# Optimization experiments

Measured on AMD Instinct MI355X. Metric: run time of the kernel, lower is better.

## Reference

```python
import jax, jax.numpy as jnp
import numpy as np

N_PRIORS = 125
N_CLASSES = 21
BATCH = 16384
THRESHOLD = 0.3
NEG_POS_RATIO = 3
ALPHA = 1.0


def setup_inputs() -> dict:
    key = jax.random.key(0)
    k1, k2, k3, k4, k5, k6, k7, k8 = jax.random.split(key, 8)
    predicted_locs = jax.random.normal(k1, (BATCH, N_PRIORS, 6), dtype=jnp.float32) * 0.1
    predicted_scores = jax.random.normal(k2, (BATCH, N_PRIORS, N_CLASSES), dtype=jnp.float32)
    # target: (N, 1, 8) = [cx, cy, w, h, angle, sin(a), cos(a), label]
    cxcy = jax.random.uniform(k3, (BATCH, 2), minval=0.2, maxval=0.8)
    wh = jax.random.uniform(k4, (BATCH, 2), minval=0.05, maxval=0.3)
    ang = jax.random.uniform(k5, (BATCH, 1), minval=-3.14159, maxval=3.14159)
    labels = jax.random.randint(k6, (BATCH, 1), 1, N_CLASSES).astype(jnp.float32)
    target = jnp.concatenate([cxcy, wh, ang, jnp.sin(ang), jnp.cos(ang), labels], axis=1)[:, None, :]
    # priors in cxcywh
    pc = jax.random.uniform(k7, (N_PRIORS, 2), minval=0.1, maxval=0.9)
    pwh = jax.random.uniform(k8, (N_PRIORS, 2), minval=0.05, maxval=0.4)
    priors_cxcy = jnp.concatenate([pc, pwh], axis=1)
    return {"predicted_locs": predicted_locs, "predicted_scores": predicted_scores,
            "target": target, "priors_cxcy": priors_cxcy}


def _iou_cxcywh(box, priors):
    # box: (4,), priors: (P,4) in (cx,cy,w,h); axis-aligned IoU
    b_lo = box[:2] - box[2:] * 0.5
    b_hi = box[:2] + box[2:] * 0.5
    p_lo = priors[:, :2] - priors[:, 2:] * 0.5
    p_hi = priors[:, :2] + priors[:, 2:] * 0.5
    inter_wh = jnp.clip(jnp.minimum(b_hi, p_hi) - jnp.maximum(b_lo, p_lo), 0.0)
    inter = inter_wh[:, 0] * inter_wh[:, 1]
    area_b = box[2] * box[3]
    area_p = priors[:, 2] * priors[:, 3]
    return inter / (area_b + area_p - inter)


def _cxcy_to_gcxgcy(cxcy, priors):
    # standard SSD encoding: cxcy (...,4) vs priors (P,4)
    g_cxcy = (cxcy[..., :2] - priors[:, :2]) / (priors[:, 2:] / 10.0)
    g_wh = jnp.log(cxcy[..., 2:] / priors[:, 2:]) * 5.0
    return jnp.concatenate([g_cxcy, g_wh], axis=-1)


def reference(predicted_locs, predicted_scores, target, priors_cxcy):
    P = priors_cxcy.shape[0]
    pred_angles = predicted_locs[..., 4:]   # (N,P,2)
    pred_locs = predicted_locs[..., :4]     # (N,P,4)

    def match(t):  # t: (1, 8), single object per image (n_objects = 1)
        box = t[0, :4]
        ov = _iou_cxcywh(box, priors_cxcy)                 # (P,)
        best_prior = jnp.argmax(ov)                        # prior_for_each_object
        ov = ov.at[best_prior].set(1.0)                    # force-match best prior
        label = jnp.where(ov < THRESHOLD, 0, t[0, 7].astype(jnp.int32))  # (P,)
        true_loc = _cxcy_to_gcxgcy(jnp.broadcast_to(box, (P, 4)), priors_cxcy)
        true_ang = jnp.broadcast_to(t[0, 5:7], (P, 2))
        return true_loc, label, true_ang

    true_locs, true_classes, true_angles = jax.vmap(match)(target)

    pos = true_classes != 0                                # (N,P)
    n_pos = pos.sum(axis=1)                                # (N,)
    n_pos_total = n_pos.sum().astype(jnp.float32)
    posf = pos.astype(jnp.float32)

    # smooth L1 (beta=1), mean over positive elements (4 coords each)
    d = pred_locs - true_locs
    sl1 = jnp.where(jnp.abs(d) < 1.0, 0.5 * d * d, jnp.abs(d) - 0.5)
    loc_loss = (sl1 * posf[..., None]).sum() / (n_pos_total * 4.0)

    # MSE over positive angle pairs, scaled by 25
    da = pred_angles - true_angles
    angle_loss = 25.0 * (da * da * posf[..., None]).sum() / (n_pos_total * 2.0)

    # per-prior cross entropy
    lse = jax.nn.logsumexp(predicted_scores, axis=-1)      # (N,P)
    picked = jnp.take_along_axis(predicted_scores, true_classes[..., None], axis=-1)[..., 0]
    conf_all = lse - picked                                # (N,P)

    conf_pos_sum = (conf_all * posf).sum()
    conf_neg = jnp.where(pos, 0.0, conf_all)
    conf_neg_sorted = -jnp.sort(-conf_neg, axis=1)         # descending
    ranks = jnp.arange(P)[None, :]
    hard = ranks < (NEG_POS_RATIO * n_pos)[:, None]
    conf_hard_neg_sum = (conf_neg_sorted * hard.astype(jnp.float32)).sum()
    conf_loss = (conf_hard_neg_sum + conf_pos_sum) / n_pos_total

    total = conf_loss + ALPHA * loc_loss + angle_loss
    return jnp.stack([conf_loss, loc_loss, angle_loss, total])
```

## Files before the change

kernel.cpp:

```cpp
#include <hip/hip_runtime.h>
#include <math.h>

#define NP 125
#define NC 21
#define ROWF (NP * NC)
#define THRESH 0.3f

__device__ inline void ald16(const float* g, float* l) {
    __builtin_amdgcn_global_load_lds(
        (const __attribute__((address_space(1))) void*)g,
        (__attribute__((address_space(3))) void*)l, 16, 0, 0);
}
__device__ inline void ald4(const float* g, float* l) {
    __builtin_amdgcn_global_load_lds(
        (const __attribute__((address_space(1))) void*)g,
        (__attribute__((address_space(3))) void*)l, 4, 0, 0);
}

__global__ void __launch_bounds__(64) mbloss_main(
    const float* __restrict__ locs, const float* __restrict__ scores,
    const float* __restrict__ target, const float* __restrict__ priors,
    float4* __restrict__ partials) {

    __shared__ float s_sc[ROWF];

    const int lane = threadIdx.x;
    const int r    = blockIdx.x;

    const float* gsc = scores + (size_t)r * ROWF;
#pragma unroll
    for (int it = 0; it < 10; ++it) {
        const int off = it * 256 + lane * 4;
        ald16(gsc + off, s_sc + off);
    }
    ald4(gsc + 2560 + lane, s_sc + 2560 + lane);
    if (lane == 0) s_sc[2624] = gsc[2624];

    const float* t = target + (size_t)r * 8;
    const float bx = t[0], by = t[1], bw = t[2], bh = t[3];
    const float sa = t[5], ca = t[6];
    const int lblT = (int)t[7];

    const int  p1 = lane + 64;
    const bool v1 = (p1 < NP);
    const float4* pr4 = (const float4*)priors;
    float4 P0 = pr4[lane];
    float4 P1 = v1 ? pr4[p1] : make_float4(0.f, 0.f, 1.f, 1.f);

    float iou0, iou1 = -1.f;
    {
        float iw = fminf(bx + bw * 0.5f, P0.x + P0.z * 0.5f) -
                   fmaxf(bx - bw * 0.5f, P0.x - P0.z * 0.5f);
        float ih = fminf(by + bh * 0.5f, P0.y + P0.w * 0.5f) -
                   fmaxf(by - bh * 0.5f, P0.y - P0.w * 0.5f);
        iw = fmaxf(iw, 0.f); ih = fmaxf(ih, 0.f);
        float inter = iw * ih;
        iou0 = inter / (bw * bh + P0.z * P0.w - inter);
    }
    if (v1) {
        float iw = fminf(bx + bw * 0.5f, P1.x + P1.z * 0.5f) -
                   fmaxf(bx - bw * 0.5f, P1.x - P1.z * 0.5f);
        float ih = fminf(by + bh * 0.5f, P1.y + P1.w * 0.5f) -
                   fmaxf(by - bh * 0.5f, P1.y - P1.w * 0.5f);
        iw = fmaxf(iw, 0.f); ih = fmaxf(ih, 0.f);
        float inter = iw * ih;
        iou1 = inter / (bw * bh + P1.z * P1.w - inter);
    }

    float bv = iou0; int bi = lane;
    if (iou1 > bv) { bv = iou1; bi = p1; }
#pragma unroll
    for (int off = 1; off < 64; off <<= 1) {
        float vo = __shfl_xor(bv, off, 64);
        int   io = __shfl_xor(bi, off, 64);
        if (vo > bv || (vo == bv && io < bi)) { bv = vo; bi = io; }
    }
    const int best = bi;

    const bool pos0 = (lane == best) || (iou0 >= THRESH);
    const bool pos1 = v1 && ((p1 == best) || (iou1 >= THRESH));
    const int npos = __popcll(__ballot(pos0)) + __popcll(__ballot(pos1));
    float acc_conf = 0.f, acc_sl1 = 0.f, acc_ang = 0.f;
    const float acc_np = (pos0 ? 1.f : 0.f) + (pos1 ? 1.f : 0.f);

#define SL1(d) (fabsf(d) < 1.f ? 0.5f * (d) * (d) : fabsf(d) - 0.5f)
    if (pos0) {
        const float* L = locs + (size_t)r * (NP * 6) + lane * 6;
        float g0 = (bx - P0.x) / (P0.z * 0.1f);
        float g1 = (by - P0.y) / (P0.w * 0.1f);
        float g2 = __logf(bw / P0.z) * 5.f;
        float g3 = __logf(bh / P0.w) * 5.f;
        float d0 = L[0] - g0, d1 = L[1] - g1, d2 = L[2] - g2, d3 = L[3] - g3;
        acc_sl1 += SL1(d0) + SL1(d1) + SL1(d2) + SL1(d3);
        float a0 = L[4] - sa, a1 = L[5] - ca;
        acc_ang += a0 * a0 + a1 * a1;
    }
    if (pos1) {
        const float* L = locs + (size_t)r * (NP * 6) + p1 * 6;
        float g0 = (bx - P1.x) / (P1.z * 0.1f);
        float g1 = (by - P1.y) / (P1.w * 0.1f);
        float g2 = __logf(bw / P1.z) * 5.f;
        float g3 = __logf(bh / P1.w) * 5.f;
        float d0 = L[0] - g0, d1 = L[1] - g1, d2 = L[2] - g2, d3 = L[3] - g3;
        acc_sl1 += SL1(d0) + SL1(d1) + SL1(d2) + SL1(d3);
        float a0 = L[4] - sa, a1 = L[5] - ca;
        acc_ang += a0 * a0 + a1 * a1;
    }

    __syncthreads();

    float conf0, conf1 = 0.f;
    {
        const float* s0 = s_sc + lane * NC;
        float m = s0[0];
#pragma unroll
        for (int c = 1; c < NC; ++c) m = fmaxf(m, s0[c]);
        float ss = 0.f;
#pragma unroll
        for (int c = 0; c < NC; ++c) ss += __expf(s0[c] - m);
        conf0 = (m + __logf(ss)) - s0[pos0 ? lblT : 0];
    }
    if (v1) {
        const float* s1 = s_sc + p1 * NC;
        float m = s1[0];
#pragma unroll
        for (int c = 1; c < NC; ++c) m = fmaxf(m, s1[c]);
        float ss = 0.f;
#pragma unroll
        for (int c = 0; c < NC; ++c) ss += __expf(s1[c] - m);
        conf1 = (m + __logf(ss)) - s1[pos1 ? lblT : 0];
    }
    if (pos0) acc_conf += conf0;
    if (pos1) acc_conf += conf1;

    float x0 = pos0 ? 0.f : conf0;
    float x1 = v1 ? (pos1 ? 0.f : conf1) : -1.f;
#pragma unroll
    for (int k = 2; k <= 128; k <<= 1) {
#pragma unroll
        for (int j = k >> 1; j >= 1; j >>= 1) {
            if (j == 64) {
                float a = fmaxf(x0, x1), b = fminf(x0, x1);
                x0 = a; x1 = b;
            } else {
                bool lower = (lane & j) == 0;
                bool d0 = ((lane & k) == 0);
                bool d1 = (((lane + 64) & k) == 0);
                float o0 = __shfl_xor(x0, j, 64);
                float o1 = __shfl_xor(x1, j, 64);
                x0 = (lower == d0) ? fmaxf(x0, o0) : fminf(x0, o0);
                x1 = (lower == d1) ? fmaxf(x1, o1) : fminf(x1, o1);
            }
        }
    }

    int kk = 3 * npos; if (kk > NP) kk = NP;
    acc_conf += (lane < kk ? x0 : 0.f) + (lane + 64 < kk ? x1 : 0.f);

    float rc = acc_conf, rs = acc_sl1, ra = acc_ang, rn = acc_np;
#pragma unroll
    for (int off = 1; off < 64; off <<= 1) {
        rc += __shfl_xor(rc, off, 64);
        rs += __shfl_xor(rs, off, 64);
        ra += __shfl_xor(ra, off, 64);
        rn += __shfl_xor(rn, off, 64);
    }
    if (lane == 0) partials[r] = make_float4(rc, rs, ra, rn);
}

__global__ void __launch_bounds__(1024) mbloss_fin(const float4* __restrict__ partials,
                                                   int n, float* __restrict__ out) {
    __shared__ float4 red[1024];
    const int tid = threadIdx.x;
    float4 a = make_float4(0.f, 0.f, 0.f, 0.f);
    for (int i = tid; i < n; i += 1024) {
        float4 p = partials[i];
        a.x += p.x; a.y += p.y; a.z += p.z; a.w += p.w;
    }
    red[tid] = a;
    __syncthreads();
    for (int s = 512; s > 0; s >>= 1) {
        if (tid < s) {
            red[tid].x += red[tid + s].x; red[tid].y += red[tid + s].y;
            red[tid].z += red[tid + s].z; red[tid].w += red[tid + s].w;
        }
        __syncthreads();
    }
    if (tid == 0) {
        float npt  = red[0].w;
        float conf = red[0].x / npt;
        float loc  = red[0].y / (npt * 4.f);
        float ang  = 25.f * red[0].z / (npt * 2.f);
        out[0] = conf; out[1] = loc; out[2] = ang; out[3] = conf + loc + ang;
    }
}

extern "C" void kernel_launch(void* const* d_in, const int* in_sizes, int n_in,
                              void* d_out, int out_size, void* d_ws, size_t ws_size,
                              hipStream_t stream) {
    const float* locs   = (const float*)d_in[0];
    const float* scores = (const float*)d_in[1];
    const float* target = (const float*)d_in[2];
    const float* priors = (const float*)d_in[3];
    float* out = (float*)d_out;

    const int batch = in_sizes[2] / 8;

    float4* partials = (float4*)d_ws;

    mbloss_main<<<batch, 64, 0, stream>>>(locs, scores, target, priors, partials);
    mbloss_fin<<<1, 1024, 0, stream>>>(partials, batch, out);
}
```

Baseline: 273.8 us.

## Split log-sum-exp into a flat per-prior kernel and batch rows per persistent wave

The single per-row kernel becomes two stages. A flat kernel with 256-thread blocks computes the log-sum-exp cross-entropy for every prior and writes two candidate conf values (for the row label and for background) to workspace. A grid-strided kernel with 2048 waves then does matching, box losses and the hard-negative sort, reading those values back. This removes the 64-thread-per-row occupancy limit and the 16384-block launch, and shrinks the final reduction to 2048 partials. In exchange it adds a round trip of an 8-byte-per-prior intermediate (about 16 MB) through global memory and one extra launch. It also assumes batch*125 is a multiple of 256, which holds for the given batch.

```diff
diff --git a/kernel.cpp b/kernel.cpp
--- a/kernel.cpp
+++ b/kernel.cpp
@@ -3,7 +3,6 @@
 
 #define NP 125
 #define NC 21
-#define ROWF (NP * NC)
 #define THRESH 0.3f
 
 __device__ inline void ald16(const float* g, float* l) {
@@ -11,35 +10,55 @@
         (const __attribute__((address_space(1))) void*)g,
         (__attribute__((address_space(3))) void*)l, 16, 0, 0);
 }
-__device__ inline void ald4(const float* g, float* l) {
-    __builtin_amdgcn_global_load_lds(
-        (const __attribute__((address_space(1))) void*)g,
-        (__attribute__((address_space(3))) void*)l, 4, 0, 0);
-}
-
-__global__ void __launch_bounds__(64) mbloss_main(
-    const float* __restrict__ locs, const float* __restrict__ scores,
-    const float* __restrict__ target, const float* __restrict__ priors,
-    float4* __restrict__ partials) {
-
-    __shared__ float s_sc[ROWF];
-
-    const int lane = threadIdx.x;
-    const int r    = blockIdx.x;
-
-    const float* gsc = scores + (size_t)r * ROWF;
-#pragma unroll
-    for (int it = 0; it < 10; ++it) {
-        const int off = it * 256 + lane * 4;
-        ald16(gsc + off, s_sc + off);
-    }
-    ald4(gsc + 2560 + lane, s_sc + 2560 + lane);
-    if (lane == 0) s_sc[2624] = gsc[2624];
-
-    const float* t = target + (size_t)r * 8;
-    const float bx = t[0], by = t[1], bw = t[2], bh = t[3];
-    const float sa = t[5], ca = t[6];
-    const int lblT = (int)t[7];
+
+__global__ void __launch_bounds__(256) mbloss_lse(
+    const float* __restrict__ scores, const float* __restrict__ target,
+    float2* __restrict__ conf2) {
+
+    __shared__ float s[256 * NC];
+
+    const int tid  = threadIdx.x;
+    const int base = blockIdx.x * 256;
+
+    const float* g = scores + (size_t)base * NC;
+#pragma unroll
+    for (int it = 0; it < 5; ++it) {
+        const int off = (it * 256 + tid) * 4;
+        ald16(g + off, s + off);
+    }
+    if (tid < 64) {
+        const int off = (5 * 256 + tid) * 4;
+        ald16(g + off, s + off);
+    }
+
+    const int idx = base + tid;
+    const int row = idx / NP;
+    const int lbl = (int)target[(size_t)row * 8 + 7];
+
+    __syncthreads();
+
+    const float* p = s + tid * NC;
+    float m = p[0];
+#pragma unroll
+    for (int c = 1; c < NC; ++c) m = fmaxf(m, p[c]);
+    float ss = 0.f;
+#pragma unroll
+    for (int c = 0; c < NC; ++c) ss += __expf(p[c] - m);
+    const float lse = m + __logf(ss);
+
+    conf2[idx] = make_float2(lse - p[lbl], lse - p[0]);
+}
+
+#define BWAVES 2048
+__global__ void __launch_bounds__(256) mbloss_row(
+    const float* __restrict__ locs, const float* __restrict__ target,
+    const float* __restrict__ priors, const float2* __restrict__ conf2,
+    float4* __restrict__ partials, int batch) {
+
+    const int tid  = threadIdx.x;
+    const int wave = tid >> 6;
+    const int lane = tid & 63;
+    const int gw   = blockIdx.x * 4 + wave;
 
     const int  p1 = lane + 64;
     const bool v1 = (p1 < NP);
@@ -47,125 +66,110 @@
     float4 P0 = pr4[lane];
     float4 P1 = v1 ? pr4[p1] : make_float4(0.f, 0.f, 1.f, 1.f);
 
-    float iou0, iou1 = -1.f;
-    {
-        float iw = fminf(bx + bw * 0.5f, P0.x + P0.z * 0.5f) -
-                   fmaxf(bx - bw * 0.5f, P0.x - P0.z * 0.5f);
-        float ih = fminf(by + bh * 0.5f, P0.y + P0.w * 0.5f) -
-                   fmaxf(by - bh * 0.5f, P0.y - P0.w * 0.5f);
-        iw = fmaxf(iw, 0.f); ih = fmaxf(ih, 0.f);
-        float inter = iw * ih;
-        iou0 = inter / (bw * bh + P0.z * P0.w - inter);
-    }
-    if (v1) {
-        float iw = fminf(bx + bw * 0.5f, P1.x + P1.z * 0.5f) -
-                   fmaxf(bx - bw * 0.5f, P1.x - P1.z * 0.5f);
-        float ih = fminf(by + bh * 0.5f, P1.y + P1.w * 0.5f) -
-                   fmaxf(by - bh * 0.5f, P1.y - P1.w * 0.5f);
-        iw = fmaxf(iw, 0.f); ih = fmaxf(ih, 0.f);
-        float inter = iw * ih;
-        iou1 = inter / (bw * bh + P1.z * P1.w - inter);
-    }
-
-    float bv = iou0; int bi = lane;
-    if (iou1 > bv) { bv = iou1; bi = p1; }
+    float acc_conf = 0.f, acc_sl1 = 0.f, acc_ang = 0.f, acc_np = 0.f;
+
+    for (int r = gw; r < batch; r += BWAVES) {
+        const float* t = target + (size_t)r * 8;
+        const float bx = t[0], by = t[1], bw = t[2], bh = t[3];
+        const float sa = t[5], ca = t[6];
+
+        float iou0, iou1 = -1.f;
+        {
+            float iw = fminf(bx + bw * 0.5f, P0.x + P0.z * 0.5f) -
+                       fmaxf(bx - bw * 0.5f, P0.x - P0.z * 0.5f);
+            float ih = fminf(by + bh * 0.5f, P0.y + P0.w * 0.5f) -
+                       fmaxf(by - bh * 0.5f, P0.y - P0.w * 0.5f);
+            iw = fmaxf(iw, 0.f); ih = fmaxf(ih, 0.f);
+            float inter = iw * ih;
+            iou0 = inter / (bw * bh + P0.z * P0.w - inter);
+        }
+        if (v1) {
+            float iw = fminf(bx + bw * 0.5f, P1.x + P1.z * 0.5f) -
+                       fmaxf(bx - bw * 0.5f, P1.x - P1.z * 0.5f);
+            float ih = fminf(by + bh * 0.5f, P1.y + P1.w * 0.5f) -
+                       fmaxf(by - bh * 0.5f, P1.y - P1.w * 0.5f);
+            iw = fmaxf(iw, 0.f); ih = fmaxf(ih, 0.f);
+            float inter = iw * ih;
+            iou1 = inter / (bw * bh + P1.z * P1.w - inter);
+        }
+
+        float2 c0 = conf2[(size_t)r * NP + lane];
+        float2 c1 = v1 ? conf2[(size_t)r * NP + p1] : make_float2(0.f, -1.f);
+
+        float bv = iou0; int bi = lane;
+        if (iou1 > bv) { bv = iou1; bi = p1; }
+#pragma unroll
+        for (int off = 1; off < 64; off <<= 1) {
+            float vo = __shfl_xor(bv, off, 64);
+            int   io = __shfl_xor(bi, off, 64);
+            if (vo > bv || (vo == bv && io < bi)) { bv = vo; bi = io; }
+        }
+        const int best = bi;
+
+        const bool pos0 = (lane == best) || (iou0 >= THRESH);
+        const bool pos1 = v1 && ((p1 == best) || (iou1 >= THRESH));
+        const int npos = __popcll(__ballot(pos0)) + __popcll(__ballot(pos1));
+        acc_np += (pos0 ? 1.f : 0.f) + (pos1 ? 1.f : 0.f);
+
+#define SL1(d) (fabsf(d) < 1.f ? 0.5f * (d) * (d) : fabsf(d) - 0.5f)
+        if (pos0) {
+            acc_conf += c0.x;
+            const float* L = locs + (size_t)r * (NP * 6) + lane * 6;
+            float g0 = (bx - P0.x) / (P0.z * 0.1f);
+            float g1 = (by - P0.y) / (P0.w * 0.1f);
+            float g2 = __logf(bw / P0.z) * 5.f;
+            float g3 = __logf(bh / P0.w) * 5.f;
+            float d0 = L[0] - g0, d1 = L[1] - g1, d2 = L[2] - g2, d3 = L[3] - g3;
+            acc_sl1 += SL1(d0) + SL1(d1) + SL1(d2) + SL1(d3);
+            float a0 = L[4] - sa, a1 = L[5] - ca;
+            acc_ang += a0 * a0 + a1 * a1;
+        }
+        if (pos1) {
+            acc_conf += c1.x;
+            const float* L = locs + (size_t)r * (NP * 6) + p1 * 6;
+            float g0 = (bx - P1.x) / (P1.z * 0.1f);
+            float g1 = (by - P1.y) / (P1.w * 0.1f);
+            float g2 = __logf(bw / P1.z) * 5.f;
+            float g3 = __logf(bh / P1.w) * 5.f;
+            float d0 = L[0] - g0, d1 = L[1] - g1, d2 = L[2] - g2, d3 = L[3] - g3;
+            acc_sl1 += SL1(d0) + SL1(d1) + SL1(d2) + SL1(d3);
+            float a0 = L[4] - sa, a1 = L[5] - ca;
+            acc_ang += a0 * a0 + a1 * a1;
+        }
+
+        float x0 = pos0 ? 0.f : c0.y;
+        float x1 = v1 ? (pos1 ? 0.f : c1.y) : -1.f;
+#pragma unroll
+        for (int k = 2; k <= 128; k <<= 1) {
+#pragma unroll
+            for (int j = k >> 1; j >= 1; j >>= 1) {
+                if (j == 64) {
+                    float a = fmaxf(x0, x1), b = fminf(x0, x1);
+                    x0 = a; x1 = b;
+                } else {
+                    bool lower = (lane & j) == 0;
+                    bool d0 = ((lane & k) == 0);
+                    bool d1 = (((lane + 64) & k) == 0);
+                    float o0 = __shfl_xor(x0, j, 64);
+                    float o1 = __shfl_xor(x1, j, 64);
+                    x0 = (lower == d0) ? fmaxf(x0, o0) : fminf(x0, o0);
+                    x1 = (lower == d1) ? fmaxf(x1, o1) : fminf(x1, o1);
+                }
+            }
+        }
+
+        int kk = 3 * npos; if (kk > NP) kk = NP;
+        acc_conf += (lane < kk ? x0 : 0.f) + (lane + 64 < kk ? x1 : 0.f);
+    }
+
 #pragma unroll
     for (int off = 1; off < 64; off <<= 1) {
-        float vo = __shfl_xor(bv, off, 64);
-        int   io = __shfl_xor(bi, off, 64);
-        if (vo > bv || (vo == bv && io < bi)) { bv = vo; bi = io; }
-    }
-    const int best = bi;
-
-    const bool pos0 = (lane == best) || (iou0 >= THRESH);
-    const bool pos1 = v1 && ((p1 == best) || (iou1 >= THRESH));
-    const int npos = __popcll(__ballot(pos0)) + __popcll(__ballot(pos1));
-    float acc_conf = 0.f, acc_sl1 = 0.f, acc_ang = 0.f;
-    const float acc_np = (pos0 ? 1.f : 0.f) + (pos1 ? 1.f : 0.f);
-
-#define SL1(d) (fabsf(d) < 1.f ? 0.5f * (d) * (d) : fabsf(d) - 0.5f)
-    if (pos0) {
-        const float* L = locs + (size_t)r * (NP * 6) + lane * 6;
-        float g0 = (bx - P0.x) / (P0.z * 0.1f);
-        float g1 = (by - P0.y) / (P0.w * 0.1f);
-        float g2 = __logf(bw / P0.z) * 5.f;
-        float g3 = __logf(bh / P0.w) * 5.f;
-        float d0 = L[0] - g0, d1 = L[1] - g1, d2 = L[2] - g2, d3 = L[3] - g3;
-        acc_sl1 += SL1(d0) + SL1(d1) + SL1(d2) + SL1(d3);
-        float a0 = L[4] - sa, a1 = L[5] - ca;
-        acc_ang += a0 * a0 + a1 * a1;
-    }
-    if (pos1) {
-        const float* L = locs + (size_t)r * (NP * 6) + p1 * 6;
-        float g0 = (bx - P1.x) / (P1.z * 0.1f);
-        float g1 = (by - P1.y) / (P1.w * 0.1f);
-        float g2 = __logf(bw / P1.z) * 5.f;
-        float g3 = __logf(bh / P1.w) * 5.f;
-        float d0 = L[0] - g0, d1 = L[1] - g1, d2 = L[2] - g2, d3 = L[3] - g3;
-        acc_sl1 += SL1(d0) + SL1(d1) + SL1(d2) + SL1(d3);
-        float a0 = L[4] - sa, a1 = L[5] - ca;
-        acc_ang += a0 * a0 + a1 * a1;
-    }
-
-    __syncthreads();
-
-    float conf0, conf1 = 0.f;
-    {
-        const float* s0 = s_sc + lane * NC;
-        float m = s0[0];
-#pragma unroll
-        for (int c = 1; c < NC; ++c) m = fmaxf(m, s0[c]);
-        float ss = 0.f;
-#pragma unroll
-        for (int c = 0; c < NC; ++c) ss += __expf(s0[c] - m);
-        conf0 = (m + __logf(ss)) - s0[pos0 ? lblT : 0];
-    }
-    if (v1) {
-        const float* s1 = s_sc + p1 * NC;
-        float m = s1[0];
-#pragma unroll
-        for (int c = 1; c < NC; ++c) m = fmaxf(m, s1[c]);
-        float ss = 0.f;
-#pragma unroll
-        for (int c = 0; c < NC; ++c) ss += __expf(s1[c] - m);
-        conf1 = (m + __logf(ss)) - s1[pos1 ? lblT : 0];
-    }
-    if (pos0) acc_conf += conf0;
-    if (pos1) acc_conf += conf1;
-
-    float x0 = pos0 ? 0.f : conf0;
-    float x1 = v1 ? (pos1 ? 0.f : conf1) : -1.f;
-#pragma unroll
-    for (int k = 2; k <= 128; k <<= 1) {
-#pragma unroll
-        for (int j = k >> 1; j >= 1; j >>= 1) {
-            if (j == 64) {
-                float a = fmaxf(x0, x1), b = fminf(x0, x1);
-                x0 = a; x1 = b;
-            } else {
-                bool lower = (lane & j) == 0;
-                bool d0 = ((lane & k) == 0);
-                bool d1 = (((lane + 64) & k) == 0);
-                float o0 = __shfl_xor(x0, j, 64);
-                float o1 = __shfl_xor(x1, j, 64);
-                x0 = (lower == d0) ? fmaxf(x0, o0) : fminf(x0, o0);
-                x1 = (lower == d1) ? fmaxf(x1, o1) : fminf(x1, o1);
-            }
-        }
-    }
-
-    int kk = 3 * npos; if (kk > NP) kk = NP;
-    acc_conf += (lane < kk ? x0 : 0.f) + (lane + 64 < kk ? x1 : 0.f);
-
-    float rc = acc_conf, rs = acc_sl1, ra = acc_ang, rn = acc_np;
-#pragma unroll
-    for (int off = 1; off < 64; off <<= 1) {
-        rc += __shfl_xor(rc, off, 64);
-        rs += __shfl_xor(rs, off, 64);
-        ra += __shfl_xor(ra, off, 64);
-        rn += __shfl_xor(rn, off, 64);
-    }
-    if (lane == 0) partials[r] = make_float4(rc, rs, ra, rn);
+        acc_conf += __shfl_xor(acc_conf, off, 64);
+        acc_sl1  += __shfl_xor(acc_sl1,  off, 64);
+        acc_ang  += __shfl_xor(acc_ang,  off, 64);
+        acc_np   += __shfl_xor(acc_np,   off, 64);
+    }
+    if (lane == 0) partials[gw] = make_float4(acc_conf, acc_sl1, acc_ang, acc_np);
 }
 
 __global__ void __launch_bounds__(1024) mbloss_fin(const float4* __restrict__ partials,
@@ -205,9 +209,13 @@
     float* out = (float*)d_out;
 
     const int batch = in_sizes[2] / 8;
-
-    float4* partials = (float4*)d_ws;
-
-    mbloss_main<<<batch, 64, 0, stream>>>(locs, scores, target, priors, partials);
-    mbloss_fin<<<1, 1024, 0, stream>>>(partials, batch, out);
-}
+    const int npri  = batch * NP;
+
+    float2* conf2    = (float2*)d_ws;
+    float4* partials = (float4*)((char*)d_ws + (size_t)npri * 8);
+
+    mbloss_lse<<<npri / 256, 256, 0, stream>>>(scores, target, conf2);
+    mbloss_row<<<BWAVES / 4, 256, 0, stream>>>(locs, target, priors, conf2,
+                                               partials, batch);
+    mbloss_fin<<<1, 1024, 0, stream>>>(partials, BWAVES, out);
+}
```

Result: slower. 291.4 us (+6.4%).

## Process two rows per wavefront with staged async LDS loads and split waitcnts

Applied to the files above, without the earlier changes.

Each 64-thread block now handles two batch rows. It issues both rows' global-to-LDS score loads up front, then uses explicit vmcnt waits so the first row's logsumexp runs while the second row is still arriving. The block-level __syncthreads is removed in favour of raw waitcnt barriers, the last score element is loaded into a register, and the loc reads use float2. Halving the block count reduces per-block launch overhead but doubles LDS per block and lowers parallelism. The hand-coded waitcnt encodings are fragile if the compiler reorders memory ops.

```diff
diff --git a/kernel.cpp b/kernel.cpp
--- a/kernel.cpp
+++ b/kernel.cpp
@@ -17,54 +17,38 @@
         (__attribute__((address_space(3))) void*)l, 4, 0, 0);
 }
 
-__global__ void __launch_bounds__(64) mbloss_main(
-    const float* __restrict__ locs, const float* __restrict__ scores,
-    const float* __restrict__ target, const float* __restrict__ priors,
-    float4* __restrict__ partials) {
-
-    __shared__ float s_sc[ROWF];
-
-    const int lane = threadIdx.x;
-    const int r    = blockIdx.x;
-
-    const float* gsc = scores + (size_t)r * ROWF;
-#pragma unroll
-    for (int it = 0; it < 10; ++it) {
-        const int off = it * 256 + lane * 4;
-        ald16(gsc + off, s_sc + off);
-    }
-    ald4(gsc + 2560 + lane, s_sc + 2560 + lane);
-    if (lane == 0) s_sc[2624] = gsc[2624];
-
-    const float* t = target + (size_t)r * 8;
-    const float bx = t[0], by = t[1], bw = t[2], bh = t[3];
-    const float sa = t[5], ca = t[6];
-    const int lblT = (int)t[7];
-
-    const int  p1 = lane + 64;
-    const bool v1 = (p1 < NP);
-    const float4* pr4 = (const float4*)priors;
-    float4 P0 = pr4[lane];
-    float4 P1 = v1 ? pr4[p1] : make_float4(0.f, 0.f, 1.f, 1.f);
+#define WAIT_VM11() do { __builtin_amdgcn_s_waitcnt(0xF7B); __builtin_amdgcn_sched_barrier(0); } while (0)
+#define WAIT_VM0()  do { __builtin_amdgcn_s_waitcnt(0xF70); __builtin_amdgcn_sched_barrier(0); } while (0)
+
+struct RowM {
+    float bx, by, bw, bh, sa, ca;
+    int   lbl, npos;
+    bool  pos0, pos1;
+};
+
+__device__ inline void match_row(const float* t, const float4& P0, const float4& P1,
+                                 int lane, int p1, bool v1, RowM& R) {
+    R.bx = t[0]; R.by = t[1]; R.bw = t[2]; R.bh = t[3];
+    R.sa = t[5]; R.ca = t[6]; R.lbl = (int)t[7];
 
     float iou0, iou1 = -1.f;
     {
-        float iw = fminf(bx + bw * 0.5f, P0.x + P0.z * 0.5f) -
-                   fmaxf(bx - bw * 0.5f, P0.x - P0.z * 0.5f);
-        float ih = fminf(by + bh * 0.5f, P0.y + P0.w * 0.5f) -
-                   fmaxf(by - bh * 0.5f, P0.y - P0.w * 0.5f);
+        float iw = fminf(R.bx + R.bw * 0.5f, P0.x + P0.z * 0.5f) -
+                   fmaxf(R.bx - R.bw * 0.5f, P0.x - P0.z * 0.5f);
+        float ih = fminf(R.by + R.bh * 0.5f, P0.y + P0.w * 0.5f) -
+                   fmaxf(R.by - R.bh * 0.5f, P0.y - P0.w * 0.5f);
         iw = fmaxf(iw, 0.f); ih = fmaxf(ih, 0.f);
         float inter = iw * ih;
-        iou0 = inter / (bw * bh + P0.z * P0.w - inter);
+        iou0 = inter / (R.bw * R.bh + P0.z * P0.w - inter);
     }
     if (v1) {
-        float iw = fminf(bx + bw * 0.5f, P1.x + P1.z * 0.5f) -
-                   fmaxf(bx - bw * 0.5f, P1.x - P1.z * 0.5f);
-        float ih = fminf(by + bh * 0.5f, P1.y + P1.w * 0.5f) -
-                   fmaxf(by - bh * 0.5f, P1.y - P1.w * 0.5f);
+        float iw = fminf(R.bx + R.bw * 0.5f, P1.x + P1.z * 0.5f) -
+                   fmaxf(R.bx - R.bw * 0.5f, P1.x - P1.z * 0.5f);
+        float ih = fminf(R.by + R.bh * 0.5f, P1.y + P1.w * 0.5f) -
+                   fmaxf(R.by - R.bh * 0.5f, P1.y - P1.w * 0.5f);
         iw = fmaxf(iw, 0.f); ih = fmaxf(ih, 0.f);
         float inter = iw * ih;
-        iou1 = inter / (bw * bh + P1.z * P1.w - inter);
+        iou1 = inter / (R.bw * R.bh + P1.z * P1.w - inter);
     }
 
     float bv = iou0; int bi = lane;
@@ -75,66 +59,48 @@
         int   io = __shfl_xor(bi, off, 64);
         if (vo > bv || (vo == bv && io < bi)) { bv = vo; bi = io; }
     }
-    const int best = bi;
-
-    const bool pos0 = (lane == best) || (iou0 >= THRESH);
-    const bool pos1 = v1 && ((p1 == best) || (iou1 >= THRESH));
-    const int npos = __popcll(__ballot(pos0)) + __popcll(__ballot(pos1));
-    float acc_conf = 0.f, acc_sl1 = 0.f, acc_ang = 0.f;
-    const float acc_np = (pos0 ? 1.f : 0.f) + (pos1 ? 1.f : 0.f);
-
-#define SL1(d) (fabsf(d) < 1.f ? 0.5f * (d) * (d) : fabsf(d) - 0.5f)
-    if (pos0) {
-        const float* L = locs + (size_t)r * (NP * 6) + lane * 6;
-        float g0 = (bx - P0.x) / (P0.z * 0.1f);
-        float g1 = (by - P0.y) / (P0.w * 0.1f);
-        float g2 = __logf(bw / P0.z) * 5.f;
-        float g3 = __logf(bh / P0.w) * 5.f;
-        float d0 = L[0] - g0, d1 = L[1] - g1, d2 = L[2] - g2, d3 = L[3] - g3;
-        acc_sl1 += SL1(d0) + SL1(d1) + SL1(d2) + SL1(d3);
-        float a0 = L[4] - sa, a1 = L[5] - ca;
-        acc_ang += a0 * a0 + a1 * a1;
-    }
-    if (pos1) {
-        const float* L = locs + (size_t)r * (NP * 6) + p1 * 6;
-        float g0 = (bx - P1.x) / (P1.z * 0.1f);
-        float g1 = (by - P1.y) / (P1.w * 0.1f);
-        float g2 = __logf(bw / P1.z) * 5.f;
-        float g3 = __logf(bh / P1.w) * 5.f;
-        float d0 = L[0] - g0, d1 = L[1] - g1, d2 = L[2] - g2, d3 = L[3] - g3;
-        acc_sl1 += SL1(d0) + SL1(d1) + SL1(d2) + SL1(d3);
-        float a0 = L[4] - sa, a1 = L[5] - ca;
-        acc_ang += a0 * a0 + a1 * a1;
-    }
-
-    __syncthreads();
-
-    float conf0, conf1 = 0.f;
-    {
-        const float* s0 = s_sc + lane * NC;
+    R.pos0 = (lane == bi) || (iou0 >= THRESH);
+    R.pos1 = v1 && ((p1 == bi) || (iou1 >= THRESH));
+    R.npos = __popcll(__ballot(R.pos0)) + __popcll(__ballot(R.pos1));
+}
+
+__device__ inline void lse_row(const float* srow, float e2624, int lane, int p1,
+                               bool v1, int sel0, int sel1,
+                               float& conf0, float& conf1) {
+    {
+        const float* s0 = srow + lane * NC;
         float m = s0[0];
 #pragma unroll
         for (int c = 1; c < NC; ++c) m = fmaxf(m, s0[c]);
-        float ss = 0.f;
-#pragma unroll
-        for (int c = 0; c < NC; ++c) ss += __expf(s0[c] - m);
-        conf0 = (m + __logf(ss)) - s0[pos0 ? lblT : 0];
-    }
+        float ss = 0.f, pick = 0.f;
+#pragma unroll
+        for (int c = 0; c < NC; ++c) {
+            ss += __expf(s0[c] - m);
+            pick += (c == sel0) ? s0[c] : 0.f;
+        }
+        conf0 = (m + __logf(ss)) - pick;
+    }
+    conf1 = 0.f;
     if (v1) {
-        const float* s1 = s_sc + p1 * NC;
-        float m = s1[0];
-#pragma unroll
-        for (int c = 1; c < NC; ++c) m = fmaxf(m, s1[c]);
-        float ss = 0.f;
-#pragma unroll
-        for (int c = 0; c < NC; ++c) ss += __expf(s1[c] - m);
-        conf1 = (m + __logf(ss)) - s1[pos1 ? lblT : 0];
-    }
-    if (pos0) acc_conf += conf0;
-    if (pos1) acc_conf += conf1;
-
-    float x0 = pos0 ? 0.f : conf0;
-    float x1 = v1 ? (pos1 ? 0.f : conf1) : -1.f;
+        const float* s1 = srow + p1 * NC;
+        const bool last = (p1 == NP - 1);
+        float m = -1e30f, ss = 0.f, pick = 0.f;
+#pragma unroll
+        for (int c = 0; c < NC; ++c) {
+            float val = (last && c == NC - 1) ? e2624 : s1[c];
+            m = fmaxf(m, val);
+        }
+#pragma unroll
+        for (int c = 0; c < NC; ++c) {
+            float val = (last && c == NC - 1) ? e2624 : s1[c];
+            ss += __expf(val - m);
+            pick += (c == sel1) ? val : 0.f;
+        }
+        conf1 = (m + __logf(ss)) - pick;
+    }
+}
+
+__device__ inline float topk_sum(float x0, float x1, int lane, int kk) {
 #pragma unroll
     for (int k = 2; k <= 128; k <<= 1) {
 #pragma unroll
@@ -153,19 +119,103 @@
             }
         }
     }
-
-    int kk = 3 * npos; if (kk > NP) kk = NP;
-    acc_conf += (lane < kk ? x0 : 0.f) + (lane + 64 < kk ? x1 : 0.f);
-
-    float rc = acc_conf, rs = acc_sl1, ra = acc_ang, rn = acc_np;
+    return (lane < kk ? x0 : 0.f) + (lane + 64 < kk ? x1 : 0.f);
+}
+
+#define SL1(d) (fabsf(d) < 1.f ? 0.5f * (d) * (d) : fabsf(d) - 0.5f)
+__device__ inline void pos_loss(const float* locs, size_t r, int p, const float4& P,
+                                const RowM& R, float& sl1, float& ang) {
+    const float2* L2 = (const float2*)(locs + r * (NP * 6) + p * 6);
+    float2 A = L2[0], B = L2[1], C = L2[2];
+    float g0 = (R.bx - P.x) / (P.z * 0.1f);
+    float g1 = (R.by - P.y) / (P.w * 0.1f);
+    float g2 = __logf(R.bw / P.z) * 5.f;
+    float g3 = __logf(R.bh / P.w) * 5.f;
+    float d0 = A.x - g0, d1 = A.y - g1, d2 = B.x - g2, d3 = B.y - g3;
+    sl1 += SL1(d0) + SL1(d1) + SL1(d2) + SL1(d3);
+    float a0 = C.x - R.sa, a1 = C.y - R.ca;
+    ang += a0 * a0 + a1 * a1;
+}
+
+__global__ void __launch_bounds__(64) mbloss_main(
+    const float* __restrict__ locs, const float* __restrict__ scores,
+    const float* __restrict__ target, const float* __restrict__ priors,
+    float4* __restrict__ partials) {
+
+    __shared__ float s_sc[2 * ROWF];
+
+    const int lane = threadIdx.x;
+    const size_t r0 = (size_t)blockIdx.x * 2;
+    const size_t r1 = r0 + 1;
+
+    const int  p1 = lane + 64;
+    const bool v1 = (p1 < NP);
+    const float4* pr4 = (const float4*)priors;
+    float4 P0 = pr4[lane];
+    float4 P1 = v1 ? pr4[p1] : make_float4(0.f, 0.f, 1.f, 1.f);
+
+    const float* g0 = scores + r0 * ROWF;
+    const float* g1 = scores + r1 * ROWF;
+    const float e0 = g0[2624];
+    const float e1 = g1[2624];
+    __builtin_amdgcn_sched_barrier(0);
+
+#pragma unroll
+    for (int it = 0; it < 10; ++it) {
+        const int off = it * 256 + lane * 4;
+        ald16(g0 + off, s_sc + off);
+    }
+    ald4(g0 + 2560 + lane, s_sc + 2560 + lane);
+#pragma unroll
+    for (int it = 0; it < 10; ++it) {
+        const int off = it * 256 + lane * 4;
+        ald16(g1 + off, s_sc + ROWF + off);
+    }
+    ald4(g1 + 2560 + lane, s_sc + ROWF + 2560 + lane);
+    __builtin_amdgcn_sched_barrier(0);
+
+    RowM R0, R1;
+    match_row(target + r0 * 8, P0, P1, lane, p1, v1, R0);
+    match_row(target + r1 * 8, P0, P1, lane, p1, v1, R1);
+
+    WAIT_VM11();
+    float c00, c01;
+    lse_row(s_sc, e0, lane, p1, v1, R0.pos0 ? R0.lbl : 0, R0.pos1 ? R0.lbl : 0, c00, c01);
+
+    WAIT_VM0();
+    float c10, c11;
+    lse_row(s_sc + ROWF, e1, lane, p1, v1, R1.pos0 ? R1.lbl : 0, R1.pos1 ? R1.lbl : 0, c10, c11);
+
+    float acc_conf = 0.f, acc_sl1 = 0.f, acc_ang = 0.f;
+    float acc_np = (R0.pos0 ? 1.f : 0.f) + (R0.pos1 ? 1.f : 0.f) +
+                   (R1.pos0 ? 1.f : 0.f) + (R1.pos1 ? 1.f : 0.f);
+
+    if (R0.pos0) { acc_conf += c00; pos_loss(locs, r0, lane, P0, R0, acc_sl1, acc_ang); }
+    if (R0.pos1) { acc_conf += c01; pos_loss(locs, r0, p1,   P1, R0, acc_sl1, acc_ang); }
+    if (R1.pos0) { acc_conf += c10; pos_loss(locs, r1, lane, P0, R1, acc_sl1, acc_ang); }
+    if (R1.pos1) { acc_conf += c11; pos_loss(locs, r1, p1,   P1, R1, acc_sl1, acc_ang); }
+
+    {
+        int kk = 3 * R0.npos; if (kk > NP) kk = NP;
+        float x0 = R0.pos0 ? 0.f : c00;
+        float x1 = v1 ? (R0.pos1 ? 0.f : c01) : -1.f;
+        acc_conf += topk_sum(x0, x1, lane, kk);
+    }
+    {
+        int kk = 3 * R1.npos; if (kk > NP) kk = NP;
+        float x0 = R1.pos0 ? 0.f : c10;
+        float x1 = v1 ? (R1.pos1 ? 0.f : c11) : -1.f;
+        acc_conf += topk_sum(x0, x1, lane, kk);
+    }
+
 #pragma unroll
     for (int off = 1; off < 64; off <<= 1) {
-        rc += __shfl_xor(rc, off, 64);
-        rs += __shfl_xor(rs, off, 64);
-        ra += __shfl_xor(ra, off, 64);
-        rn += __shfl_xor(rn, off, 64);
-    }
-    if (lane == 0) partials[r] = make_float4(rc, rs, ra, rn);
+        acc_conf += __shfl_xor(acc_conf, off, 64);
+        acc_sl1  += __shfl_xor(acc_sl1,  off, 64);
+        acc_ang  += __shfl_xor(acc_ang,  off, 64);
+        acc_np   += __shfl_xor(acc_np,   off, 64);
+    }
+    if (lane == 0) partials[blockIdx.x] = make_float4(acc_conf, acc_sl1, acc_ang, acc_np);
 }
 
 __global__ void __launch_bounds__(1024) mbloss_fin(const float4* __restrict__ partials,
@@ -205,9 +255,10 @@
     float* out = (float*)d_out;
 
     const int batch = in_sizes[2] / 8;
+    const int nblk  = batch / 2;
 
     float4* partials = (float4*)d_ws;
 
-    mbloss_main<<<batch, 64, 0, stream>>>(locs, scores, target, priors, partials);
-    mbloss_fin<<<1, 1024, 0, stream>>>(partials, batch, out);
-}
+    mbloss_main<<<nblk, 64, 0, stream>>>(locs, scores, target, priors, partials);
+    mbloss_fin<<<1, 1024, 0, stream>>>(partials, nblk, out);
+}
```

Measured after the change: 276.6 us. Within noise of the previous version (+1.0%).
